# Kernel tuning notes

Measured on AMD Instinct MI355X. Metric: run time of the kernel, lower is better.

Reference implementation:

```python
import jax, jax.numpy as jnp
import numpy as np

# Static config (matches init_kwargs / chosen geometry)
DIM, HEADS, WS, SHIFT = 96, 3, 7, 3
H, W = 56, 56
B = 64
N = WS * WS
HID = int(DIM * 4.0)
EPS = 1e-5


def _rel_tables():
    # relative_coords_table: (1, 2*WS-1, 2*WS-1, 2), log-spaced coords in [-1,1]
    c = np.arange(-(WS - 1), WS, dtype=np.float32)
    tab = np.stack(np.meshgrid(c, c, indexing='ij'), axis=-1)[None]
    tab = tab / (WS - 1) * 8.0
    tab = np.sign(tab) * np.log2(np.abs(tab) + 1.0) / np.log2(8.0)
    # relative_position_index: (N, N) int
    coords = np.stack(np.meshgrid(np.arange(WS), np.arange(WS), indexing='ij'))
    cf = coords.reshape(2, -1)
    rel = (cf[:, :, None] - cf[:, None, :]).transpose(1, 2, 0).astype(np.int64)
    rel[..., 0] += WS - 1
    rel[..., 1] += WS - 1
    rel[..., 0] *= 2 * WS - 1
    return jnp.asarray(tab), jnp.asarray(rel.sum(-1))

_TABLE, _RPI = _rel_tables()


def _shift_mask():
    # standard SW-MSA mask: (num_windows, N, N), 0 / -100
    img = np.zeros((1, H, W, 1), dtype=np.float32)
    cnt = 0
    segs = (slice(0, -WS), slice(-WS, -SHIFT), slice(-SHIFT, None))
    for hs in segs:
        for ws_ in segs:
            img[:, hs, ws_, :] = cnt
            cnt += 1
    mw = img.reshape(1, H // WS, WS, W // WS, WS, 1).transpose(0, 1, 3, 2, 4, 5).reshape(-1, N)
    am = mw[:, None, :] - mw[:, :, None]
    return jnp.asarray(np.where(am != 0, -100.0, 0.0).astype(np.float32))


def _ln(x, g, b):
    mu = x.mean(-1, keepdims=True)
    var = x.var(-1, keepdims=True)
    return (x - mu) * jax.lax.rsqrt(var + EPS) * g + b


def setup_inputs() -> dict:
    key = jax.random.key(0)
    ks = jax.random.split(key, 8)
    s = 0.02
    return {
        'x': jax.random.normal(ks[0], (B, H * W, DIM), jnp.float32),
        'attn_mask': _shift_mask(),
        'qkv_w': jax.random.normal(ks[1], (3 * DIM, DIM), jnp.float32) * s,
        'q_bias': jnp.zeros((DIM,), jnp.float32),
        'v_bias': jnp.zeros((DIM,), jnp.float32),
        'logit_scale': jnp.full((HEADS, 1, 1), np.log(10.0), jnp.float32),
        'cpb_w1': jax.random.normal(ks[2], (512, 2), jnp.float32) * s,
        'cpb_b1': jnp.zeros((512,), jnp.float32),
        'cpb_w2': jax.random.normal(ks[3], (HEADS, 512), jnp.float32) * s,
        'proj_w': jax.random.normal(ks[4], (DIM, DIM), jnp.float32) * s,
        'proj_b': jnp.zeros((DIM,), jnp.float32),
        'norm1_g': jnp.ones((DIM,), jnp.float32),
        'norm1_b': jnp.zeros((DIM,), jnp.float32),
        'fc1_w': jax.random.normal(ks[5], (HID, DIM), jnp.float32) * s,
        'fc1_b': jnp.zeros((HID,), jnp.float32),
        'fc2_w': jax.random.normal(ks[6], (DIM, HID), jnp.float32) * s,
        'fc2_b': jnp.zeros((DIM,), jnp.float32),
        'norm2_g': jnp.ones((DIM,), jnp.float32),
        'norm2_b': jnp.zeros((DIM,), jnp.float32),
    }


def reference(x, attn_mask, qkv_w, q_bias, v_bias, logit_scale, cpb_w1, cpb_b1,
              cpb_w2, proj_w, proj_b, norm1_g, norm1_b, fc1_w, fc1_b, fc2_w,
              fc2_b, norm2_g, norm2_b):
    Bx, L, C = x.shape
    d = C // HEADS
    nH, nWd = H // WS, W // WS
    shortcut = x

    xi = x.reshape(Bx, H, W, C)
    xi = jnp.roll(xi, (-SHIFT, -SHIFT), axis=(1, 2))
    # window partition -> (Bx*nH*nWd, N, C)
    xw = xi.reshape(Bx, nH, WS, nWd, WS, C).transpose(0, 1, 3, 2, 4, 5).reshape(-1, N, C)

    # qkv with q/v bias only (k bias fixed to zero)
    qkv_bias = jnp.concatenate([q_bias, jnp.zeros_like(v_bias), v_bias])
    qkv = (xw @ qkv_w.T + qkv_bias).reshape(-1, N, 3, HEADS, d).transpose(2, 0, 3, 1, 4)
    q, k, v = qkv[0], qkv[1], qkv[2]  # (B_, h, N, d)

    # cosine attention with clamped learnable temperature
    qn = q / jnp.maximum(jnp.linalg.norm(q, axis=-1, keepdims=True), 1e-12)
    kn = k / jnp.maximum(jnp.linalg.norm(k, axis=-1, keepdims=True), 1e-12)
    attn = jnp.einsum('bhnd,bhmd->bhnm', qn, kn)
    scale = jnp.exp(jnp.minimum(logit_scale, jnp.log(jnp.float32(100.0))))
    attn = attn * scale

    # continuous relative position bias via cpb_mlp
    tab = jax.nn.gelu(_TABLE @ cpb_w1.T + cpb_b1, approximate=False) @ cpb_w2.T
    tab = tab.reshape(-1, HEADS)
    rpb = tab[_RPI.reshape(-1)].reshape(N, N, HEADS).transpose(2, 0, 1)
    attn = attn + (16.0 * jax.nn.sigmoid(rpb))[None]

    # shift mask
    nWin = attn_mask.shape[0]
    attn = attn.reshape(-1, nWin, HEADS, N, N) + attn_mask[None, :, None]
    attn = jax.nn.softmax(attn.reshape(-1, HEADS, N, N), axis=-1)

    out = jnp.einsum('bhnm,bhmd->bnhd', attn, v).reshape(-1, N, C)
    out = out @ proj_w.T + proj_b

    # window reverse + un-shift
    out = out.reshape(Bx, nH, nWd, WS, WS, C).transpose(0, 1, 3, 2, 4, 5).reshape(Bx, H, W, C)
    out = jnp.roll(out, (SHIFT, SHIFT), axis=(1, 2)).reshape(Bx, L, C)

    # SwinV2 post-norm residuals
    x1 = shortcut + _ln(out, norm1_g, norm1_b)
    h = jax.nn.gelu(x1 @ fc1_w.T + fc1_b, approximate=False) @ fc2_w.T + fc2_b
    return x1 + _ln(h, norm2_g, norm2_b)
```

## Files before the change

kernel.cpp:

```cpp
#include <hip/hip_runtime.h>
#include <math.h>

#define BATCH 64
#define HW 56
#define CDIM 96
#define NHEADS 3
#define WSZ 7
#define NTOK 49
#define SHIFT_ 3
#define NWIN_TOT 4096
#define HID 384
#define NTOKENS (BATCH * HW * HW)
#define LN100 4.6051702f

typedef __attribute__((ext_vector_type(8))) short bf16x8;
typedef __attribute__((ext_vector_type(8))) _Float16 f16x8;
typedef __attribute__((ext_vector_type(4))) float f32x4;

__device__ inline f32x4 mfma16(bf16x8 a, bf16x8 b, f32x4 c) {
  return __builtin_amdgcn_mfma_f32_16x16x32_bf16(a, b, c, 0, 0, 0);
}
__device__ inline f32x4 mfma16h(f16x8 a, f16x8 b, f32x4 c) {
  return __builtin_amdgcn_mfma_f32_16x16x32_f16(a, b, c, 0, 0, 0);
}

__device__ inline unsigned short f2b(float f) {
  unsigned u = __float_as_uint(f);
  unsigned r = (u + 0x7FFFu + ((u >> 16) & 1u)) >> 16;
  return (unsigned short)r;
}
__device__ inline float blo(unsigned u) { return __uint_as_float(u << 16); }
__device__ inline float bhi(unsigned u) { return __uint_as_float(u & 0xFFFF0000u); }
__device__ inline unsigned packb(float a, float b) {
  return (unsigned)f2b(a) | ((unsigned)f2b(b) << 16);
}
__device__ inline unsigned packh(float a, float b) {
  _Float16 ha = (_Float16)a, hb = (_Float16)b;
  unsigned short ua = *(unsigned short*)&ha, ub = *(unsigned short*)&hb;
  return (unsigned)ua | ((unsigned)ub << 16);
}
__device__ inline float gelu_f(float v) {
  float a = fabsf(v) * 0.70710678118654752f;
  float t = 1.0f / fmaf(a, 0.3275911f, 1.0f);
  float p = t * fmaf(t, fmaf(t, fmaf(t, fmaf(t, 1.061405429f, -1.453152027f),
                                     1.421413741f), -0.284496736f), 0.254829592f);
  float er = 1.0f - p * __expf(-a * a);
  er = (v < 0.f) ? -er : er;
  return 0.5f * v * (1.0f + er);
}

__global__ __launch_bounds__(256) void wconv2_kernel(
    const float* __restrict__ qkv_w, const float* __restrict__ fc1_w,
    const float* __restrict__ fc2_w, const float* __restrict__ proj_w,
    unsigned* __restrict__ qkvf, unsigned* __restrict__ w1f,
    unsigned* __restrict__ w2f, unsigned* __restrict__ pwf) {
  int T = blockIdx.x * 256 + threadIdx.x;
  if (T < 3456) {
    int tk = T >> 6, l = T & 63;
    int n = tk / 3, ks = tk - n * 3;
    int o = n * 16 + (l & 15);
    const float* src = qkv_w + o * 96 + ks * 32 + (l >> 4) * 8;
    uint4 d;
    d.x = packb(src[0], src[1]); d.y = packb(src[2], src[3]);
    d.z = packb(src[4], src[5]); d.w = packb(src[6], src[7]);
    *(uint4*)&qkvf[(size_t)(tk * 64 + l) * 4] = d;
    return;
  }
  T -= 3456;
  if (T < 4608) {
    int tk = T >> 6, l = T & 63;
    int n = tk / 3, ks = tk - n * 3;
    int o = n * 16 + (l & 15);
    const float* src = fc1_w + o * 96 + ks * 32 + (l >> 4) * 8;
    uint4 d;
    d.x = packb(src[0], src[1]); d.y = packb(src[2], src[3]);
    d.z = packb(src[4], src[5]); d.w = packb(src[6], src[7]);
    *(uint4*)&w1f[(size_t)(tk * 64 + l) * 4] = d;
    return;
  }
  T -= 4608;
  if (T < 4608) {
    int tk = T >> 6, l = T & 63;
    int n = tk / 12, ks = tk - n * 12;
    int o = n * 16 + (l & 15);
    const float* src = fc2_w + o * 384 + ks * 32 + (l >> 4) * 8;
    uint4 d;
    d.x = packb(src[0], src[1]); d.y = packb(src[2], src[3]);
    d.z = packb(src[4], src[5]); d.w = packb(src[6], src[7]);
    *(uint4*)&w2f[(size_t)(tk * 64 + l) * 4] = d;
    return;
  }
  T -= 4608;
  if (T < 1152) {
    int tk = T >> 6, l = T & 63;
    int n = tk / 3, ks = tk - n * 3;
    int o = n * 16 + (l & 15);
    const float* src = proj_w + o * 96 + ks * 32 + (l >> 4) * 8;
    uint4 d;
    d.x = packb(src[0], src[1]); d.y = packb(src[2], src[3]);
    d.z = packb(src[4], src[5]); d.w = packb(src[6], src[7]);
    *(uint4*)&pwf[(size_t)(tk * 64 + l) * 4] = d;
  }
}

__global__ __launch_bounds__(512) void cpb_table_kernel(
    const float* __restrict__ w1, const float* __restrict__ b1,
    const float* __restrict__ w2, float* __restrict__ tabout) {
  int tid = threadIdx.x;
  if (tid >= 169 * 3) return;
  int e = tid / 3, h = tid - e * 3;
  int i = e / 13, j = e - i * 13;
  float ti = (float)(i - 6) * (8.0f / 6.0f);
  float tj = (float)(j - 6) * (8.0f / 6.0f);
  float sx = (ti > 0.f) ? 1.f : (ti < 0.f ? -1.f : 0.f);
  float sy = (tj > 0.f) ? 1.f : (tj < 0.f ? -1.f : 0.f);
  float tx = sx * log2f(fabsf(ti) + 1.f) * (1.0f / 3.0f);
  float ty = sy * log2f(fabsf(tj) + 1.f) * (1.0f / 3.0f);
  float acc = 0.f;
  for (int jj = 0; jj < 512; ++jj) {
    float hv = tx * w1[jj * 2 + 0] + ty * w1[jj * 2 + 1] + b1[jj];
    float g = 0.5f * hv * (1.f + erff(hv * 0.70710678118654752f));
    acc += g * w2[h * 512 + jj];
  }
  tabout[e * 3 + h] = acc;
}

__global__ __launch_bounds__(256) void bias_kernel(
    const float* __restrict__ tabout, float* __restrict__ bias16) {
  int idx = blockIdx.x * 256 + threadIdx.x;
  if (idx >= NHEADS * NTOK * NTOK) return;
  int h = idx / (NTOK * NTOK);
  int rem = idx - h * NTOK * NTOK;
  int i = rem / NTOK, j = rem - i * NTOK;
  int ri = (i / WSZ) - (j / WSZ) + 6;
  int ci = (i % WSZ) - (j % WSZ) + 6;
  int e = ri * 13 + ci;
  float v = tabout[e * 3 + h];
  bias16[idx] = 16.f / (1.f + expf(-v));
}

__global__ __launch_bounds__(256) void qkv_mfma_kernel(
    const float* __restrict__ x, const unsigned* __restrict__ qkvf,
    const float* __restrict__ q_bias, const float* __restrict__ v_bias,
    const float* __restrict__ logit_scale,
    unsigned* __restrict__ qws, unsigned* __restrict__ kws,
    unsigned* __restrict__ vws) {
  __shared__ unsigned xa[64 * 52];
  int tid = threadIdx.x, lane = tid & 63, wv = tid >> 6;
  size_t tok0 = (size_t)blockIdx.x * 64;

  for (int idx = tid; idx < 3072; idx += 256) {
    int t = idx / 48, c2 = idx - t * 48;
    const float2 s = *(const float2*)(x + (tok0 + t) * 96 + c2 * 2);
    xa[t * 52 + c2] = packb(s.x, s.y);
  }
  __syncthreads();

  int c15 = lane & 15, q4 = lane >> 4;
  bf16x8 afr[3];
  #pragma unroll
  for (int k = 0; k < 3; ++k)
    afr[k] = *(const bf16x8*)&xa[(wv * 16 + c15) * 52 + k * 16 + q4 * 4];

  f32x4 acc[18];
  #pragma unroll
  for (int n = 0; n < 18; ++n) acc[n] = f32x4{0.f, 0.f, 0.f, 0.f};
  #pragma unroll
  for (int n = 0; n < 18; ++n) {
    #pragma unroll
    for (int k = 0; k < 3; ++k) {
      bf16x8 b = *(const bf16x8*)&qkvf[(size_t)((n * 3 + k) * 64 + lane) * 4];
      acc[n] = mfma16(afr[k], b, acc[n]);
    }
  }

  int tokr0 = (int)tok0 + wv * 16 + q4 * 4;
  int wbase[4];
  #pragma unroll
  for (int i = 0; i < 4; ++i) {
    int tk = tokr0 + i;
    int bb = tk / 3136, rem = tk - bb * 3136;
    int R = rem / 56, C = rem - R * 56;
    int rr = R + 53; if (rr >= 56) rr -= 56;
    int cc = C + 53; if (cc >= 56) cc -= 56;
    int wr = rr / 7, tr2 = rr - wr * 7;
    int wc = cc / 7, tc2 = cc - wc * 7;
    wbase[i] = (bb * 64 + wr * 8 + wc) * 2352 + (tr2 * 7 + tc2) * 16;
  }

  #pragma unroll
  for (int h = 0; h < 3; ++h) {
    float sc = expf(fminf(logit_scale[h], LN100));
    {
      f32x4 a0 = acc[2 * h], a1 = acc[2 * h + 1];
      float b0 = q_bias[h * 32 + c15], b1 = q_bias[h * 32 + 16 + c15];
      unsigned pk[8];
      #pragma unroll
      for (int i = 0; i < 4; ++i) {
        float va = a0[i] + b0, vb = a1[i] + b1;
        float ss = va * va + vb * vb;
        ss += __shfl_xor(ss, 1, 64); ss += __shfl_xor(ss, 2, 64);
        ss += __shfl_xor(ss, 4, 64); ss += __shfl_xor(ss, 8, 64);
        float inv = sc / fmaxf(sqrtf(ss), 1e-12f);
        va *= inv; vb *= inv;
        float pa = __shfl_xor(va, 1, 64), pb = __shfl_xor(vb, 1, 64);
        pk[i] = packb(va, pa); pk[4 + i] = packb(vb, pb);
      }
      if (!(lane & 1)) {
        int dw0 = c15 >> 1;
        #pragma unroll
        for (int i = 0; i < 4; ++i) {
          size_t base = (size_t)wbase[i] + h * 784;
          qws[base + dw0] = pk[i];
          qws[base + 8 + dw0] = pk[4 + i];
        }
      }
    }
    {
      f32x4 a0 = acc[6 + 2 * h], a1 = acc[7 + 2 * h];
      unsigned pk[8];
      #pragma unroll
      for (int i = 0; i < 4; ++i) {
        float va = a0[i], vb = a1[i];
        float ss = va * va + vb * vb;
        ss += __shfl_xor(ss, 1, 64); ss += __shfl_xor(ss, 2, 64);
        ss += __shfl_xor(ss, 4, 64); ss += __shfl_xor(ss, 8, 64);
        float inv = 1.f / fmaxf(sqrtf(ss), 1e-12f);
        va *= inv; vb *= inv;
        float pa = __shfl_xor(va, 1, 64), pb = __shfl_xor(vb, 1, 64);
        pk[i] = packb(va, pa); pk[4 + i] = packb(vb, pb);
      }
      if (!(lane & 1)) {
        int dw0 = c15 >> 1;
        #pragma unroll
        for (int i = 0; i < 4; ++i) {
          size_t base = (size_t)wbase[i] + h * 784;
          kws[base + dw0] = pk[i];
          kws[base + 8 + dw0] = pk[4 + i];
        }
      }
    }
    {
      f32x4 a0 = acc[12 + 2 * h], a1 = acc[13 + 2 * h];
      float b0 = v_bias[h * 32 + c15], b1 = v_bias[h * 32 + 16 + c15];
      unsigned pk[8];
      #pragma unroll
      for (int i = 0; i < 4; ++i) {
        float va = a0[i] + b0, vb = a1[i] + b1;
        float pa = __shfl_xor(va, 1, 64), pb = __shfl_xor(vb, 1, 64);
        pk[i] = packb(va, pa); pk[4 + i] = packb(vb, pb);
      }
      if (!(lane & 1)) {
        int dw0 = c15 >> 1;
        #pragma unroll
        for (int i = 0; i < 4; ++i) {
          size_t base = (size_t)wbase[i] + h * 784;
          vws[base + dw0] = pk[i];
          vws[base + 8 + dw0] = pk[4 + i];
        }
      }
    }
  }
}

__global__ __launch_bounds__(256) void attn_fused_kernel(
    const unsigned* __restrict__ qws, const unsigned* __restrict__ kws,
    const unsigned* __restrict__ vws, const float* __restrict__ bias16,
    const float* __restrict__ mask, const unsigned* __restrict__ pwf,
    const float* __restrict__ proj_b, const float* __restrict__ x,
    const float* __restrict__ n1g, const float* __restrict__ n1b,
    float* __restrict__ out) {
  __shared__ __align__(16) unsigned smem[10368];
  _Float16* VtS  = (_Float16*)smem;
  unsigned* obuf = (unsigned*)smem;
  _Float16* Ph   = (_Float16*)((char*)smem + 13824);
  unsigned* Phd  = (unsigned*)((char*)smem + 13824);
  float*    ybuf = (float*)((char*)smem + 13824);

  int tid = threadIdx.x, lane = tid & 63, wv = tid >> 6;
  int c15 = lane & 15, q4 = lane >> 4;
  int win = blockIdx.x;
  int b = win >> 6, wi = win & 63, wh = wi >> 3, wcx = wi & 7;
  size_t wroot = (size_t)win * 2352;

  bf16x8 qf[4], kf[4];
  if (wv < 3) {
    size_t wb = wroot + (size_t)wv * 784;
    #pragma unroll
    for (int m = 0; m < 4; ++m) {
      int t = m * 16 + c15; if (t > 48) t = 48;
      qf[m] = *(const bf16x8*)&qws[wb + t * 16 + q4 * 4];
    }
    #pragma unroll
    for (int n = 0; n < 4; ++n) {
      int t = n * 16 + c15; if (t > 48) t = 48;
      kf[n] = *(const bf16x8*)&kws[wb + t * 16 + q4 * 4];
    }
  }

  for (int idx = tid; idx < 768; idx += 256) {
    int h2 = idx >> 8, rem = idx & 255;
    int t = rem >> 2, dg = rem & 3;
    int tc2 = t > 48 ? 48 : t;
    uint4 v4 = *(const uint4*)&vws[wroot + h2 * 784 + tc2 * 16 + dg * 4];
    _Float16* dst = &VtS[h2 * 2304 + (dg * 8) * 72 + t];
    dst[0 * 72] = (_Float16)blo(v4.x); dst[1 * 72] = (_Float16)bhi(v4.x);
    dst[2 * 72] = (_Float16)blo(v4.y); dst[3 * 72] = (_Float16)bhi(v4.y);
    dst[4 * 72] = (_Float16)blo(v4.z); dst[5 * 72] = (_Float16)bhi(v4.z);
    dst[6 * 72] = (_Float16)blo(v4.w); dst[7 * 72] = (_Float16)bhi(v4.w);
  }
  __syncthreads();

  f32x4 o[4][2];
  #pragma unroll
  for (int m = 0; m < 4; ++m)
    #pragma unroll
    for (int n2 = 0; n2 < 2; ++n2) o[m][n2] = f32x4{0.f, 0.f, 0.f, 0.f};

  if (wv < 3) {
    int h = wv;
    f32x4 s[4][4];
    #pragma unroll
    for (int m = 0; m < 4; ++m)
      #pragma unroll
      for (int n = 0; n < 4; ++n)
        s[m][n] = mfma16(qf[m], kf[n], f32x4{0.f, 0.f, 0.f, 0.f});

    const float* bsl = bias16 + h * 2401;
    const float* msl = mask + (size_t)wi * 2401;
    #pragma unroll
    for (int m = 0; m < 4; ++m) {
      #pragma unroll
      for (int i = 0; i < 4; ++i) {
        int rw = m * 16 + 4 * q4 + i;
        if (rw < 49) {
          const float* br = bsl + rw * 49;
          const float* mr = msl + rw * 49;
          #pragma unroll
          for (int n = 0; n < 4; ++n) {
            int j = n * 16 + c15;
            s[m][n][i] = (j < 49) ? (s[m][n][i] + br[j] + mr[j]) : -1e30f;
          }
        } else {
          #pragma unroll
          for (int n = 0; n < 4; ++n)
            if (n * 16 + c15 >= 49) s[m][n][i] = -1e30f;
        }
      }
    }

    #pragma unroll
    for (int m = 0; m < 4; ++m) {
      #pragma unroll
      for (int i = 0; i < 4; ++i) {
        float mx = fmaxf(fmaxf(s[m][0][i], s[m][1][i]), fmaxf(s[m][2][i], s[m][3][i]));
        mx = fmaxf(mx, __shfl_xor(mx, 1, 64)); mx = fmaxf(mx, __shfl_xor(mx, 2, 64));
        mx = fmaxf(mx, __shfl_xor(mx, 4, 64)); mx = fmaxf(mx, __shfl_xor(mx, 8, 64));
        float sum = 0.f;
        #pragma unroll
        for (int n = 0; n < 4; ++n) { float e = __expf(s[m][n][i] - mx); s[m][n][i] = e; sum += e; }
        sum += __shfl_xor(sum, 1, 64); sum += __shfl_xor(sum, 2, 64);
        sum += __shfl_xor(sum, 4, 64); sum += __shfl_xor(sum, 8, 64);
        float inv = 1.f / sum;
        #pragma unroll
        for (int n = 0; n < 4; ++n) s[m][n][i] *= inv;
      }
    }

    #pragma unroll
    for (int m = 0; m < 4; ++m)
      #pragma unroll
      for (int n = 0; n < 4; ++n)
        #pragma unroll
        for (int i = 0; i < 4; ++i) {
          float pv = s[m][n][i];
          float pn = __shfl_xor(pv, 1, 64);
          if (!(lane & 1)) {
            int row = m * 16 + 4 * q4 + i;
            Phd[h * 2304 + row * 36 + n * 8 + (c15 >> 1)] = packh(pv, pn);
          }
        }
    asm volatile("s_waitcnt lgkmcnt(0)" ::: "memory");
    __builtin_amdgcn_sched_barrier(0);

    #pragma unroll
    for (int ks = 0; ks < 2; ++ks) {
      f16x8 pa[4];
      #pragma unroll
      for (int m = 0; m < 4; ++m)
        pa[m] = *(const f16x8*)&Ph[h * 4608 + (m * 16 + c15) * 72 + ks * 32 + q4 * 8];
      #pragma unroll
      for (int n2 = 0; n2 < 2; ++n2) {
        f16x8 vb = *(const f16x8*)&VtS[h * 2304 + (n2 * 16 + c15) * 72 + ks * 32 + q4 * 8];
        #pragma unroll
        for (int m = 0; m < 4; ++m) o[m][n2] = mfma16h(pa[m], vb, o[m][n2]);
      }
    }
  }
  __syncthreads();

  if (wv < 3) {
    int h = wv;
    #pragma unroll
    for (int m = 0; m < 4; ++m)
      #pragma unroll
      for (int n2 = 0; n2 < 2; ++n2)
        #pragma unroll
        for (int i = 0; i < 4; ++i) {
          float ov = o[m][n2][i];
          float on = __shfl_xor(ov, 1, 64);
          if (!(lane & 1))
            obuf[(m * 16 + 4 * q4 + i) * 52 + h * 16 + n2 * 8 + (c15 >> 1)] = packb(ov, on);
        }
  }
  __syncthreads();

  bf16x8 oa[3];
  #pragma unroll
  for (int ks = 0; ks < 3; ++ks)
    oa[ks] = *(const bf16x8*)&obuf[(wv * 16 + c15) * 52 + ks * 16 + q4 * 4];
  f32x4 pr[6];
  #pragma unroll
  for (int n = 0; n < 6; ++n) pr[n] = f32x4{0.f, 0.f, 0.f, 0.f};
  #pragma unroll
  for (int n = 0; n < 6; ++n)
    #pragma unroll
    for (int ks = 0; ks < 3; ++ks) {
      bf16x8 bfr = *(const bf16x8*)&pwf[(size_t)((n * 3 + ks) * 64 + lane) * 4];
      pr[n] = mfma16(oa[ks], bfr, pr[n]);
    }

  #pragma unroll
  for (int n = 0; n < 6; ++n) {
    int col = n * 16 + c15;
    float bo = proj_b[col];
    #pragma unroll
    for (int i = 0; i < 4; ++i)
      ybuf[(wv * 16 + 4 * q4 + i) * 100 + col] = pr[n][i] + bo;
  }
  __syncthreads();

  int t = tid >> 2, pp = tid & 3;
  if (t < 49) {
    const float* yrow = ybuf + t * 100 + pp * 24;
    float s1 = 0.f;
    #pragma unroll
    for (int c = 0; c < 24; ++c) s1 += yrow[c];
    s1 += __shfl_xor(s1, 1, 64); s1 += __shfl_xor(s1, 2, 64);
    float mu = s1 * (1.f / 96.f);
    float v2 = 0.f;
    #pragma unroll
    for (int c = 0; c < 24; ++c) { float d = yrow[c] - mu; v2 += d * d; }
    v2 += __shfl_xor(v2, 1, 64); v2 += __shfl_xor(v2, 2, 64);
    float rs = rsqrtf(v2 * (1.f / 96.f) + 1e-5f);
    int tr = (t * 9363) >> 16, tc = t - tr * 7;
    int R = wh * 7 + tr + SHIFT_; if (R >= HW) R -= HW;
    int C = wcx * 7 + tc + SHIFT_; if (C >= HW) C -= HW;
    size_t base = ((size_t)(b * 3136 + R * 56 + C)) * 96 + pp * 24;
    #pragma unroll
    for (int c4 = 0; c4 < 6; ++c4) {
      float4 xv = *(const float4*)(x + base + c4 * 4);
      float4 gv = *(const float4*)(n1g + pp * 24 + c4 * 4);
      float4 bv = *(const float4*)(n1b + pp * 24 + c4 * 4);
      float4 ov;
      ov.x = xv.x + (yrow[c4 * 4 + 0] - mu) * rs * gv.x + bv.x;
      ov.y = xv.y + (yrow[c4 * 4 + 1] - mu) * rs * gv.y + bv.y;
      ov.z = xv.z + (yrow[c4 * 4 + 2] - mu) * rs * gv.z + bv.z;
      ov.w = xv.w + (yrow[c4 * 4 + 3] - mu) * rs * gv.w + bv.w;
      *(float4*)(out + base + c4 * 4) = ov;
    }
  }
}

__global__ __launch_bounds__(256) void mlp_mfma_kernel(
    const unsigned* __restrict__ w1f, const float* __restrict__ fc1_b,
    const unsigned* __restrict__ w2f, const float* __restrict__ fc2_b,
    const float* __restrict__ n2g, const float* __restrict__ n2b,
    float* __restrict__ xio) {
  __shared__ unsigned xa[64 * 52];
  __shared__ unsigned hid[64 * 196];
  __shared__ float mu_s[64], rs_s[64];
  int tid = threadIdx.x, lane = tid & 63, wv = tid >> 6;
  int c15 = lane & 15, q4 = lane >> 4;
  size_t tok0 = (size_t)blockIdx.x * 64;

  for (int idx = tid; idx < 3072; idx += 256) {
    int t = idx / 48, c2 = idx - t * 48;
    const float2 s = *(const float2*)(xio + (tok0 + t) * 96 + c2 * 2);
    xa[t * 52 + c2] = packb(s.x, s.y);
  }
  __syncthreads();

  bf16x8 afr[4][3];
  #pragma unroll
  for (int m = 0; m < 4; ++m)
    #pragma unroll
    for (int k = 0; k < 3; ++k)
      afr[m][k] = *(const bf16x8*)&xa[(m * 16 + c15) * 52 + k * 16 + q4 * 4];
  f32x4 acc[4][6];
  #pragma unroll
  for (int m = 0; m < 4; ++m)
    #pragma unroll
    for (int n = 0; n < 6; ++n) acc[m][n] = f32x4{0.f, 0.f, 0.f, 0.f};
  #pragma unroll
  for (int n = 0; n < 6; ++n) {
    #pragma unroll
    for (int k = 0; k < 3; ++k) {
      bf16x8 b = *(const bf16x8*)&w1f[(size_t)(((6 * wv + n) * 3 + k) * 64 + lane) * 4];
      #pragma unroll
      for (int m = 0; m < 4; ++m) acc[m][n] = mfma16(afr[m][k], b, acc[m][n]);
    }
  }
  unsigned short* hidb = (unsigned short*)hid;
  #pragma unroll
  for (int n = 0; n < 6; ++n) {
    int col = (6 * wv + n) * 16 + c15;
    float bo = fc1_b[col];
    #pragma unroll
    for (int m = 0; m < 4; ++m) {
      #pragma unroll
      for (int i = 0; i < 4; ++i) {
        float g = gelu_f(acc[m][n][i] + bo);
        hidb[(m * 16 + q4 * 4 + i) * 392 + col] = f2b(g);
      }
    }
  }
  __syncthreads();

  f32x4 acc2[6];
  #pragma unroll
  for (int n = 0; n < 6; ++n) acc2[n] = f32x4{0.f, 0.f, 0.f, 0.f};
  #pragma unroll
  for (int k = 0; k < 12; ++k) {
    bf16x8 a = *(const bf16x8*)&hid[(wv * 16 + c15) * 196 + k * 16 + q4 * 4];
    #pragma unroll
    for (int n = 0; n < 6; ++n) {
      bf16x8 b = *(const bf16x8*)&w2f[(size_t)((n * 12 + k) * 64 + lane) * 4];
      acc2[n] = mfma16(a, b, acc2[n]);
    }
  }
  __syncthreads();

  float* ybuf = (float*)hid;
  #pragma unroll
  for (int n = 0; n < 6; ++n) {
    int col = n * 16 + c15;
    float bo = fc2_b[col];
    #pragma unroll
    for (int i = 0; i < 4; ++i)
      ybuf[(wv * 16 + q4 * 4 + i) * 100 + col] = acc2[n][i] + bo;
  }
  __syncthreads();

  {
    int t = tid >> 2, p = tid & 3;
    const float* row = ybuf + t * 100 + p * 24;
    float s = 0.f, s2 = 0.f;
    for (int c = 0; c < 24; ++c) { float v = row[c]; s += v; s2 += v * v; }
    s += __shfl_xor(s, 1, 64); s2 += __shfl_xor(s2, 1, 64);
    s += __shfl_xor(s, 2, 64); s2 += __shfl_xor(s2, 2, 64);
    if (p == 0) {
      float mu = s * (1.f / 96.f);
      float var = s2 * (1.f / 96.f) - mu * mu;
      mu_s[t] = mu;
      rs_s[t] = rsqrtf(fmaxf(var, 0.f) + 1e-5f);
    }
  }
  __syncthreads();

  for (int idx = tid; idx < 1536; idx += 256) {
    int t = idx / 24, c4 = (idx - t * 24) * 4;
    float mu = mu_s[t], rs = rs_s[t];
    float4 y4 = *(float4*)&ybuf[t * 100 + c4];
    float4 g4 = *(const float4*)&n2g[c4];
    float4 b4 = *(const float4*)&n2b[c4];
    float* gp = &xio[tok0 * 96 + t * 96 + c4];
    float4 x4 = *(const float4*)gp;
    float4 ov;
    ov.x = x4.x + (y4.x - mu) * rs * g4.x + b4.x;
    ov.y = x4.y + (y4.y - mu) * rs * g4.y + b4.y;
    ov.z = x4.z + (y4.z - mu) * rs * g4.z + b4.z;
    ov.w = x4.w + (y4.w - mu) * rs * g4.w + b4.w;
    *(float4*)gp = ov;
  }
}

extern "C" void kernel_launch(void* const* d_in, const int* in_sizes, int n_in,
                              void* d_out, int out_size, void* d_ws, size_t ws_size,
                              hipStream_t stream) {
  const float* x           = (const float*)d_in[0];
  const float* attn_mask   = (const float*)d_in[1];
  const float* qkv_w       = (const float*)d_in[2];
  const float* q_bias      = (const float*)d_in[3];
  const float* v_bias      = (const float*)d_in[4];
  const float* logit_scale = (const float*)d_in[5];
  const float* cpb_w1      = (const float*)d_in[6];
  const float* cpb_b1      = (const float*)d_in[7];
  const float* cpb_w2      = (const float*)d_in[8];
  const float* proj_w      = (const float*)d_in[9];
  const float* proj_b      = (const float*)d_in[10];
  const float* n1g         = (const float*)d_in[11];
  const float* n1b         = (const float*)d_in[12];
  const float* fc1_w       = (const float*)d_in[13];
  const float* fc1_b       = (const float*)d_in[14];
  const float* fc2_w       = (const float*)d_in[15];
  const float* fc2_b       = (const float*)d_in[16];
  const float* n2g         = (const float*)d_in[17];
  const float* n2b         = (const float*)d_in[18];
  float* out = (float*)d_out;

  float* tab     = (float*)d_ws;
  float* bias16  = tab + 512;
  unsigned* qkvf = (unsigned*)(bias16 + 7296);
  unsigned* w1f  = qkvf + 13824;
  unsigned* w2f  = w1f + 18432;
  unsigned* pwf  = w2f + 18432;
  unsigned* qws  = pwf + 4608;
  unsigned* kws  = qws + 9633792;
  unsigned* vws  = kws + 9633792;

  wconv2_kernel<<<54, 256, 0, stream>>>(qkv_w, fc1_w, fc2_w, proj_w,
                                        qkvf, w1f, w2f, pwf);
  cpb_table_kernel<<<1, 512, 0, stream>>>(cpb_w1, cpb_b1, cpb_w2, tab);
  bias_kernel<<<(NHEADS * NTOK * NTOK + 255) / 256, 256, 0, stream>>>(tab, bias16);
  qkv_mfma_kernel<<<NTOKENS / 64, 256, 0, stream>>>(x, qkvf, q_bias, v_bias,
                                                    logit_scale, qws, kws, vws);
  attn_fused_kernel<<<NWIN_TOT, 256, 0, stream>>>(qws, kws, vws, bias16, attn_mask,
                                                  pwf, proj_b, x, n1g, n1b, out);
  mlp_mfma_kernel<<<NTOKENS / 64, 256, 0, stream>>>(w1f, fc1_b, w2f, fc2_b,
                                                    n2g, n2b, out);
}
```

Measured before the change: 478.3 us.

## Spread attention row-tiles over all four waves and premerge bias with mask

The attention kernel previously ran the QK/softmax/PV stage on only three of four waves, one head per wave with four row tiles each. Now the 12 (head, row-tile) units are split three per wave, so every wave works and each holds fewer score registers. The relative-position bias and the shift mask are combined once into a per-window, per-head table, so the kernel does one load per score instead of two. The tradeoff is a larger precomputed table (about 1.8 MB) and each wave reloading K fragments for every unit it handles.

```diff
diff --git a/kernel.cpp b/kernel.cpp
--- a/kernel.cpp
+++ b/kernel.cpp
@@ -125,18 +125,20 @@
   tabout[e * 3 + h] = acc;
 }
 
-__global__ __launch_bounds__(256) void bias_kernel(
-    const float* __restrict__ tabout, float* __restrict__ bias16) {
+__global__ __launch_bounds__(256) void bm_kernel(
+    const float* __restrict__ tabout, const float* __restrict__ mask,
+    float* __restrict__ bmtab) {
   int idx = blockIdx.x * 256 + threadIdx.x;
-  if (idx >= NHEADS * NTOK * NTOK) return;
-  int h = idx / (NTOK * NTOK);
-  int rem = idx - h * NTOK * NTOK;
-  int i = rem / NTOK, j = rem - i * NTOK;
+  if (idx >= 64 * NHEADS * NTOK * NTOK) return;
+  int wi = idx / (NHEADS * 2401);
+  int rem = idx - wi * (NHEADS * 2401);
+  int h = rem / 2401, ij = rem - h * 2401;
+  int i = ij / NTOK, j = ij - i * NTOK;
   int ri = (i / WSZ) - (j / WSZ) + 6;
   int ci = (i % WSZ) - (j % WSZ) + 6;
   int e = ri * 13 + ci;
   float v = tabout[e * 3 + h];
-  bias16[idx] = 16.f / (1.f + expf(-v));
+  bmtab[idx] = 16.f / (1.f + expf(-v)) + mask[(size_t)wi * 2401 + ij];
 }
 
 __global__ __launch_bounds__(256) void qkv_mfma_kernel(
@@ -265,11 +267,10 @@
 
 __global__ __launch_bounds__(256) void attn_fused_kernel(
     const unsigned* __restrict__ qws, const unsigned* __restrict__ kws,
-    const unsigned* __restrict__ vws, const float* __restrict__ bias16,
-    const float* __restrict__ mask, const unsigned* __restrict__ pwf,
-    const float* __restrict__ proj_b, const float* __restrict__ x,
-    const float* __restrict__ n1g, const float* __restrict__ n1b,
-    float* __restrict__ out) {
+    const unsigned* __restrict__ vws, const float* __restrict__ bmtab,
+    const unsigned* __restrict__ pwf, const float* __restrict__ proj_b,
+    const float* __restrict__ x, const float* __restrict__ n1g,
+    const float* __restrict__ n1b, float* __restrict__ out) {
   __shared__ __align__(16) unsigned smem[10368];
   _Float16* VtS  = (_Float16*)smem;
   unsigned* obuf = (unsigned*)smem;
@@ -282,21 +283,6 @@
   int win = blockIdx.x;
   int b = win >> 6, wi = win & 63, wh = wi >> 3, wcx = wi & 7;
   size_t wroot = (size_t)win * 2352;
-
-  bf16x8 qf[4], kf[4];
-  if (wv < 3) {
-    size_t wb = wroot + (size_t)wv * 784;
-    #pragma unroll
-    for (int m = 0; m < 4; ++m) {
-      int t = m * 16 + c15; if (t > 48) t = 48;
-      qf[m] = *(const bf16x8*)&qws[wb + t * 16 + q4 * 4];
-    }
-    #pragma unroll
-    for (int n = 0; n < 4; ++n) {
-      int t = n * 16 + c15; if (t > 48) t = 48;
-      kf[n] = *(const bf16x8*)&kws[wb + t * 16 + q4 * 4];
-    }
-  }
 
   for (int idx = tid; idx < 768; idx += 256) {
     int h2 = idx >> 8, rem = idx & 255;
@@ -311,107 +297,104 @@
   }
   __syncthreads();
 
-  f32x4 o[4][2];
-  #pragma unroll
-  for (int m = 0; m < 4; ++m)
-    #pragma unroll
-    for (int n2 = 0; n2 < 2; ++n2) o[m][n2] = f32x4{0.f, 0.f, 0.f, 0.f};
-
-  if (wv < 3) {
-    int h = wv;
-    f32x4 s[4][4];
-    #pragma unroll
-    for (int m = 0; m < 4; ++m)
-      #pragma unroll
-      for (int n = 0; n < 4; ++n)
-        s[m][n] = mfma16(qf[m], kf[n], f32x4{0.f, 0.f, 0.f, 0.f});
-
-    const float* bsl = bias16 + h * 2401;
-    const float* msl = mask + (size_t)wi * 2401;
-    #pragma unroll
-    for (int m = 0; m < 4; ++m) {
+  f32x4 oall[3][2];
+  #pragma unroll
+  for (int t = 0; t < 3; ++t)
+    #pragma unroll
+    for (int n2 = 0; n2 < 2; ++n2) oall[t][n2] = f32x4{0.f, 0.f, 0.f, 0.f};
+
+  #pragma unroll
+  for (int t = 0; t < 3; ++t) {
+    int id = wv * 3 + t;
+    int h = id >> 2, mm = id & 3;
+    size_t wb = wroot + (size_t)h * 784;
+
+    int tq = mm * 16 + c15; if (tq > 48) tq = 48;
+    bf16x8 qf = *(const bf16x8*)&qws[wb + tq * 16 + q4 * 4];
+    bf16x8 kf[4];
+    #pragma unroll
+    for (int n = 0; n < 4; ++n) {
+      int tk = n * 16 + c15; if (tk > 48) tk = 48;
+      kf[n] = *(const bf16x8*)&kws[wb + tk * 16 + q4 * 4];
+    }
+
+    f32x4 s[4];
+    #pragma unroll
+    for (int n = 0; n < 4; ++n)
+      s[n] = mfma16(qf, kf[n], f32x4{0.f, 0.f, 0.f, 0.f});
+
+    const float* bm = bmtab + ((size_t)wi * 3 + h) * 2401;
+    #pragma unroll
+    for (int i = 0; i < 4; ++i) {
+      int rw = mm * 16 + 4 * q4 + i;
+      if (rw < 49) {
+        const float* br = bm + rw * 49;
+        #pragma unroll
+        for (int n = 0; n < 4; ++n) {
+          int j = n * 16 + c15;
+          s[n][i] = (j < 49) ? (s[n][i] + br[j]) : -1e30f;
+        }
+      } else {
+        #pragma unroll
+        for (int n = 0; n < 4; ++n)
+          if (n * 16 + c15 >= 49) s[n][i] = -1e30f;
+      }
+    }
+
+    #pragma unroll
+    for (int i = 0; i < 4; ++i) {
+      float mx = fmaxf(fmaxf(s[0][i], s[1][i]), fmaxf(s[2][i], s[3][i]));
+      mx = fmaxf(mx, __shfl_xor(mx, 1, 64)); mx = fmaxf(mx, __shfl_xor(mx, 2, 64));
+      mx = fmaxf(mx, __shfl_xor(mx, 4, 64)); mx = fmaxf(mx, __shfl_xor(mx, 8, 64));
+      float sum = 0.f;
+      #pragma unroll
+      for (int n = 0; n < 4; ++n) { float e = __expf(s[n][i] - mx); s[n][i] = e; sum += e; }
+      sum += __shfl_xor(sum, 1, 64); sum += __shfl_xor(sum, 2, 64);
+      sum += __shfl_xor(sum, 4, 64); sum += __shfl_xor(sum, 8, 64);
+      float inv = 1.f / sum;
+      #pragma unroll
+      for (int n = 0; n < 4; ++n) s[n][i] *= inv;
+    }
+
+    #pragma unroll
+    for (int n = 0; n < 4; ++n)
       #pragma unroll
       for (int i = 0; i < 4; ++i) {
-        int rw = m * 16 + 4 * q4 + i;
-        if (rw < 49) {
-          const float* br = bsl + rw * 49;
-          const float* mr = msl + rw * 49;
-          #pragma unroll
-          for (int n = 0; n < 4; ++n) {
-            int j = n * 16 + c15;
-            s[m][n][i] = (j < 49) ? (s[m][n][i] + br[j] + mr[j]) : -1e30f;
-          }
-        } else {
-          #pragma unroll
-          for (int n = 0; n < 4; ++n)
-            if (n * 16 + c15 >= 49) s[m][n][i] = -1e30f;
+        float pv = s[n][i];
+        float pn = __shfl_xor(pv, 1, 64);
+        if (!(lane & 1)) {
+          int row = mm * 16 + 4 * q4 + i;
+          Phd[h * 2304 + row * 36 + n * 8 + (c15 >> 1)] = packh(pv, pn);
         }
       }
-    }
-
-    #pragma unroll
-    for (int m = 0; m < 4; ++m) {
-      #pragma unroll
-      for (int i = 0; i < 4; ++i) {
-        float mx = fmaxf(fmaxf(s[m][0][i], s[m][1][i]), fmaxf(s[m][2][i], s[m][3][i]));
-        mx = fmaxf(mx, __shfl_xor(mx, 1, 64)); mx = fmaxf(mx, __shfl_xor(mx, 2, 64));
-        mx = fmaxf(mx, __shfl_xor(mx, 4, 64)); mx = fmaxf(mx, __shfl_xor(mx, 8, 64));
-        float sum = 0.f;
-        #pragma unroll
-        for (int n = 0; n < 4; ++n) { float e = __expf(s[m][n][i] - mx); s[m][n][i] = e; sum += e; }
-        sum += __shfl_xor(sum, 1, 64); sum += __shfl_xor(sum, 2, 64);
-        sum += __shfl_xor(sum, 4, 64); sum += __shfl_xor(sum, 8, 64);
-        float inv = 1.f / sum;
-        #pragma unroll
-        for (int n = 0; n < 4; ++n) s[m][n][i] *= inv;
-      }
-    }
-
-    #pragma unroll
-    for (int m = 0; m < 4; ++m)
-      #pragma unroll
-      for (int n = 0; n < 4; ++n)
-        #pragma unroll
-        for (int i = 0; i < 4; ++i) {
-          float pv = s[m][n][i];
-          float pn = __shfl_xor(pv, 1, 64);
-          if (!(lane & 1)) {
-            int row = m * 16 + 4 * q4 + i;
-            Phd[h * 2304 + row * 36 + n * 8 + (c15 >> 1)] = packh(pv, pn);
-          }
-        }
     asm volatile("s_waitcnt lgkmcnt(0)" ::: "memory");
     __builtin_amdgcn_sched_barrier(0);
 
     #pragma unroll
     for (int ks = 0; ks < 2; ++ks) {
-      f16x8 pa[4];
-      #pragma unroll
-      for (int m = 0; m < 4; ++m)
-        pa[m] = *(const f16x8*)&Ph[h * 4608 + (m * 16 + c15) * 72 + ks * 32 + q4 * 8];
+      f16x8 pa = *(const f16x8*)&Ph[h * 4608 + (mm * 16 + c15) * 72 + ks * 32 + q4 * 8];
       #pragma unroll
       for (int n2 = 0; n2 < 2; ++n2) {
         f16x8 vb = *(const f16x8*)&VtS[h * 2304 + (n2 * 16 + c15) * 72 + ks * 32 + q4 * 8];
-        #pragma unroll
-        for (int m = 0; m < 4; ++m) o[m][n2] = mfma16h(pa[m], vb, o[m][n2]);
-      }
-    }
-  }
-  __syncthreads();
-
-  if (wv < 3) {
-    int h = wv;
-    #pragma unroll
-    for (int m = 0; m < 4; ++m)
-      #pragma unroll
-      for (int n2 = 0; n2 < 2; ++n2)
-        #pragma unroll
-        for (int i = 0; i < 4; ++i) {
-          float ov = o[m][n2][i];
-          float on = __shfl_xor(ov, 1, 64);
-          if (!(lane & 1))
-            obuf[(m * 16 + 4 * q4 + i) * 52 + h * 16 + n2 * 8 + (c15 >> 1)] = packb(ov, on);
-        }
+        oall[t][n2] = mfma16h(pa, vb, oall[t][n2]);
+      }
+    }
+  }
+  __syncthreads();
+
+  #pragma unroll
+  for (int t = 0; t < 3; ++t) {
+    int id = wv * 3 + t;
+    int h = id >> 2, mm = id & 3;
+    #pragma unroll
+    for (int n2 = 0; n2 < 2; ++n2)
+      #pragma unroll
+      for (int i = 0; i < 4; ++i) {
+        float ov = oall[t][n2][i];
+        float on = __shfl_xor(ov, 1, 64);
+        if (!(lane & 1))
+          obuf[(mm * 16 + 4 * q4 + i) * 52 + h * 16 + n2 * 8 + (c15 >> 1)] = packb(ov, on);
+      }
   }
   __syncthreads();
 
@@ -610,8 +593,8 @@
   float* out = (float*)d_out;
 
   float* tab     = (float*)d_ws;
-  float* bias16  = tab + 512;
-  unsigned* qkvf = (unsigned*)(bias16 + 7296);
+  float* bmtab   = tab + 512;
+  unsigned* qkvf = (unsigned*)(bmtab + 460992);
   unsigned* w1f  = qkvf + 13824;
   unsigned* w2f  = w1f + 18432;
   unsigned* pwf  = w2f + 18432;
@@ -622,10 +605,11 @@
   wconv2_kernel<<<54, 256, 0, stream>>>(qkv_w, fc1_w, fc2_w, proj_w,
                                         qkvf, w1f, w2f, pwf);
   cpb_table_kernel<<<1, 512, 0, stream>>>(cpb_w1, cpb_b1, cpb_w2, tab);
-  bias_kernel<<<(NHEADS * NTOK * NTOK + 255) / 256, 256, 0, stream>>>(tab, bias16);
+  bm_kernel<<<(64 * NHEADS * NTOK * NTOK + 255) / 256, 256, 0, stream>>>(
+      tab, attn_mask, bmtab);
   qkv_mfma_kernel<<<NTOKENS / 64, 256, 0, stream>>>(x, qkvf, q_bias, v_bias,
                                                     logit_scale, qws, kws, vws);
-  attn_fused_kernel<<<NWIN_TOT, 256, 0, stream>>>(qws, kws, vws, bias16, attn_mask,
+  attn_fused_kernel<<<NWIN_TOT, 256, 0, stream>>>(qws, kws, vws, bmtab,
                                                   pwf, proj_b, x, n1g, n1b, out);
   mlp_mfma_kernel<<<NTOKENS / 64, 256, 0, stream>>>(w1f, fc1_b, w2f, fc2_b,
                                                     n2g, n2b, out);
```

Result: faster. 438.7 us (median of 4 runs) (-8.3%).
